# Kernel optimization log

Hardware: AMD Instinct MI355X
Metric: run time of the kernel (lower is better)

Reference implementation:

```python
import jax, jax.numpy as jnp
import numpy as np

B, Q, K, C, H = 4, 1024, 1024, 1024, 16
L = C            # latent_dim (== in_dim per module construction)
CH = L // H      # head_dim = 64


def _ln(x, w, b):
    m = jnp.mean(x, -1, keepdims=True)
    v = jnp.mean((x - m) ** 2, -1, keepdims=True)
    return (x - m) * jax.lax.rsqrt(v + 1e-5) * w + b


def setup_inputs() -> dict:
    key = jax.random.key(0)
    ks = jax.random.split(key, 16)
    s = 0.02
    return {
        "queries": jax.random.normal(ks[0], (B, Q, C), jnp.float32),
        "contexts": jax.random.normal(ks[1], (B, K, C), jnp.float32),
        "queries_hidden": jax.random.normal(ks[2], (B, Q, L), jnp.float32),
        "sa_norm_w": jnp.ones((C,), jnp.float32),
        "sa_norm_b": jnp.zeros((C,), jnp.float32),
        "sa_qkv_w": jax.random.normal(ks[3], (C, 2 * L + C), jnp.float32) * s,
        "sa_out_w": jax.random.normal(ks[4], (C, C), jnp.float32) * s,
        "sa_out_b": jnp.zeros((C,), jnp.float32),
        "ca_norm_w": jnp.ones((C,), jnp.float32),
        "ca_norm_b": jnp.zeros((C,), jnp.float32),
        "gru_w_ih": jax.random.normal(ks[5], (3 * L, C), jnp.float32) * s,
        "gru_w_hh": jax.random.normal(ks[6], (3 * L, L), jnp.float32) * s,
        "gru_b_ih": jnp.zeros((3 * L,), jnp.float32),
        "gru_b_hh": jnp.zeros((3 * L,), jnp.float32),
        "ca_k_w": jax.random.normal(ks[7], (C, L), jnp.float32) * s,
        "ca_v_w": jax.random.normal(ks[8], (C, C), jnp.float32) * s,
        "ca_out_w": jax.random.normal(ks[9], (C, C), jnp.float32) * s,
        "ca_out_b": jnp.zeros((C,), jnp.float32),
        "ln1_w": jnp.ones((C,), jnp.float32),
        "ln1_b": jnp.zeros((C,), jnp.float32),
        "lin1_w": jax.random.normal(ks[10], (C, 2 * C), jnp.float32) * s,
        "ln2_w": jnp.ones((2 * C,), jnp.float32),
        "ln2_b": jnp.zeros((2 * C,), jnp.float32),
        "lin2_w": jax.random.normal(ks[11], (2 * C, C), jnp.float32) * s,
    }


def reference(queries, contexts, queries_hidden,
              sa_norm_w, sa_norm_b, sa_qkv_w, sa_out_w, sa_out_b,
              ca_norm_w, ca_norm_b, gru_w_ih, gru_w_hh, gru_b_ih, gru_b_hh,
              ca_k_w, ca_v_w, ca_out_w, ca_out_b,
              ln1_w, ln1_b, lin1_w, ln2_w, ln2_b, lin2_w):
    scale = 1.0 / jnp.sqrt(jnp.asarray(C, queries.dtype))

    # ---- SelfAttention (pre-norm, residual) ----
    xn = _ln(queries, sa_norm_w, sa_norm_b)
    qkv = (xn @ sa_qkv_w).reshape(B, Q, H, -1)          # [B,Q,H, 2*CH + C/H]
    q, k, v = jnp.split(qkv, [CH, 2 * CH], axis=-1)
    e = jnp.einsum('nqhc,nkhc->nhqk', q, k) * scale
    a = jax.nn.softmax(e, axis=-1)
    o = jnp.einsum('nhqk,nkhc->nqhc', a, v).reshape(B, Q, C)
    x = o @ sa_out_w + sa_out_b + queries

    # ---- AttentionDynamicQuery (GRU-updated queries, cross-attn) ----
    x_pre = x
    xn = _ln(x, ca_norm_w, ca_norm_b)
    xf = xn.reshape(B * Q, C)
    hf = queries_hidden.reshape(B * Q, L)
    gi = xf @ gru_w_ih.T + gru_b_ih                     # [BQ, 3L]
    gh = hf @ gru_w_hh.T + gru_b_hh
    gir, giz, gin = jnp.split(gi, 3, axis=-1)
    ghr, ghz, ghn = jnp.split(gh, 3, axis=-1)
    r = jax.nn.sigmoid(gir + ghr)
    z = jax.nn.sigmoid(giz + ghz)
    n = jnp.tanh(gin + r * ghn)
    h = (1.0 - z) * n + z * hf                          # PyTorch GRUCell update
    qh = h.reshape(B, Q, H, CH)                         # new queries_hidden

    kk = (contexts @ ca_k_w).reshape(B, K, H, CH)
    vv = (contexts @ ca_v_w).reshape(B, K, H, C // H)
    energy = jnp.einsum('nqhc,nkhc->nhqk', qh, kk)      # returned UNscaled
    att = jax.nn.softmax(energy * scale, axis=-1)
    o = jnp.einsum('nhqk,nkhc->nqhc', att, vv).reshape(B, Q, C)
    x = o @ ca_out_w + ca_out_b + x_pre

    # ---- MLP: LN -> SiLU -> Linear -> LN -> SiLU -> Linear, residual ----
    m = jax.nn.silu(_ln(x, ln1_w, ln1_b)) @ lin1_w
    m = jax.nn.silu(_ln(m, ln2_w, ln2_b)) @ lin2_w
    out = x + m                                         # dropout(p=0) = identity
    return (out, energy, qh)
```

## Files before the change

kernel.cpp:

```cpp
#include <hip/hip_runtime.h>
#include <hip/hip_bf16.h>
#include <math.h>

static constexpr float SCALE = 0.03125f;

typedef __attribute__((ext_vector_type(4))) float f32x4;
typedef __attribute__((ext_vector_type(8))) __bf16 bf16x8;
typedef __attribute__((ext_vector_type(4))) __bf16 bf16x4;

__device__ __forceinline__ void g2l16(const void* g, void* l) {
  __builtin_amdgcn_global_load_lds(
      (const __attribute__((address_space(1))) unsigned int*)g,
      (__attribute__((address_space(3))) unsigned int*)l,
      16, 0, 0);
}

__global__ __launch_bounds__(256) void prep_all(
    const float* __restrict__ sa_qkv_w, const float* __restrict__ ca_k_w,
    const float* __restrict__ ca_v_w, const float* __restrict__ sa_out_w,
    const float* __restrict__ ca_out_w, const float* __restrict__ lin1_w,
    const float* __restrict__ lin2_w, const float* __restrict__ gru_w_ih,
    const float* __restrict__ gru_w_hh, const float* __restrict__ qhid,
    const float* __restrict__ contexts,
    __bf16* __restrict__ qkvT, __bf16* __restrict__ kT, __bf16* __restrict__ vT,
    __bf16* __restrict__ saoT, __bf16* __restrict__ caoT, __bf16* __restrict__ lin1T,
    __bf16* __restrict__ lin2T, __bf16* __restrict__ ihB, __bf16* __restrict__ hhB,
    __bf16* __restrict__ qhB, __bf16* __restrict__ ctxB) {
  int bid = blockIdx.x;
  int t = threadIdx.x;
  if (bid >= 2816) {
    const float* csrc; __bf16* cdst; int cbase;
    if (bid < 4352)      { csrc = gru_w_ih; cdst = ihB;  cbase = 2816; }
    else if (bid < 5888) { csrc = gru_w_hh; cdst = hhB;  cbase = 4352; }
    else if (bid < 7936) { csrc = qhid;     cdst = qhB;  cbase = 5888; }
    else                 { csrc = contexts; cdst = ctxB; cbase = 7936; }
    size_t idx = ((size_t)(bid - cbase) * 256 + t) * 8;
    float4 a = *(const float4*)(csrc + idx);
    float4 b = *(const float4*)(csrc + idx + 4);
    bf16x8 o = {(__bf16)a.x,(__bf16)a.y,(__bf16)a.z,(__bf16)a.w,
                (__bf16)b.x,(__bf16)b.y,(__bf16)b.z,(__bf16)b.w};
    *(bf16x8*)(cdst + idx) = o;
    return;
  }
  const float* src; __bf16* dst; int Kd, N, base;
  if (bid < 768)       { src = sa_qkv_w; dst = qkvT;  Kd = 1024; N = 3072; base = 0; }
  else if (bid < 1024) { src = ca_k_w;   dst = kT;    Kd = 1024; N = 1024; base = 768; }
  else if (bid < 1280) { src = ca_v_w;   dst = vT;    Kd = 1024; N = 1024; base = 1024; }
  else if (bid < 1536) { src = sa_out_w; dst = saoT;  Kd = 1024; N = 1024; base = 1280; }
  else if (bid < 1792) { src = ca_out_w; dst = caoT;  Kd = 1024; N = 1024; base = 1536; }
  else if (bid < 2304) { src = lin1_w;   dst = lin1T; Kd = 1024; N = 2048; base = 1792; }
  else                 { src = lin2_w;   dst = lin2T; Kd = 2048; N = 1024; base = 2304; }
  int tid = bid - base;
  int ntx = N >> 6;
  int n0 = (tid % ntx) * 64, k0 = (tid / ntx) * 64;
  __shared__ float tile[64][65];
  #pragma unroll
  for (int i = 0; i < 16; ++i) {
    int idx = i * 256 + t; int r = idx >> 6, c = idx & 63;
    tile[r][c] = src[(size_t)(k0 + r) * N + n0 + c];
  }
  __syncthreads();
  #pragma unroll
  for (int i = 0; i < 16; ++i) {
    int idx = i * 256 + t; int r = idx >> 6, c = idx & 63;
    dst[(size_t)(n0 + r) * Kd + k0 + c] = (__bf16)tile[c][r];
  }
}

template <int NV>
__global__ __launch_bounds__(256) void ln_bf16(
    const float* __restrict__ xf, const __bf16* __restrict__ xb,
    const float* __restrict__ w, const float* __restrict__ b,
    __bf16* __restrict__ out, int silu) {
  const int D = NV * 1024;
  int row = blockIdx.x, t = threadIdx.x;
  float vals[NV * 4];
  float s = 0.f, s2 = 0.f;
  #pragma unroll
  for (int i = 0; i < NV; ++i) {
    int c = (i * 256 + t) * 4;
    float4 v;
    if (xf) {
      v = *(const float4*)(xf + (size_t)row * D + c);
    } else {
      bf16x4 vb = *(const bf16x4*)(xb + (size_t)row * D + c);
      v = make_float4((float)vb[0], (float)vb[1], (float)vb[2], (float)vb[3]);
    }
    vals[i*4+0] = v.x; vals[i*4+1] = v.y; vals[i*4+2] = v.z; vals[i*4+3] = v.w;
    s += v.x + v.y + v.z + v.w;
    s2 += v.x*v.x + v.y*v.y + v.z*v.z + v.w*v.w;
  }
  #pragma unroll
  for (int off = 32; off > 0; off >>= 1) {
    s += __shfl_xor(s, off);
    s2 += __shfl_xor(s2, off);
  }
  __shared__ float red[4], red2[4];
  int wv = t >> 6;
  if ((t & 63) == 0) { red[wv] = s; red2[wv] = s2; }
  __syncthreads();
  float S  = red[0] + red[1] + red[2] + red[3];
  float S2 = red2[0] + red2[1] + red2[2] + red2[3];
  float mean = S / D;
  float var = S2 / D - mean * mean;
  float rs = rsqrtf(var + 1e-5f);
  #pragma unroll
  for (int i = 0; i < NV; ++i) {
    int c = (i * 256 + t) * 4;
    bf16x4 o;
    #pragma unroll
    for (int j = 0; j < 4; ++j) {
      float v = (vals[i*4+j] - mean) * rs * w[c+j] + b[c+j];
      if (silu) v = v / (1.f + __expf(-v));
      o[j] = (__bf16)v;
    }
    *(bf16x4*)(out + (size_t)row * D + c) = o;
  }
}

__device__ __forceinline__ void gemm_body(
    __bf16* Asm, __bf16* Bsm,
    const __bf16* __restrict__ A, long long lda,
    const __bf16* __restrict__ B, long long ldb,
    float* __restrict__ outF, __bf16* __restrict__ outB, long long ldc,
    const float* __restrict__ bias, const float* __restrict__ res,
    int K, int bm, int bn) {
  int t = threadIdx.x;
  int lane = t & 63, w = t >> 6;
  int l15 = lane & 15, kg = lane >> 4;
  int wm = (w >> 1) * 64, wn = (w & 1) * 64;

  f32x4 acc[4][4];
  #pragma unroll
  for (int i = 0; i < 4; ++i)
    #pragma unroll
    for (int j = 0; j < 4; ++j) acc[i][j] = (f32x4)(0.0f);

  const __bf16* ga[4]; const __bf16* gb[4];
  __bf16* la[4]; __bf16* lb[4];
  #pragma unroll
  for (int i = 0; i < 4; ++i) {
    int slot = i * 256 + t;
    int row = slot >> 3, s = slot & 7;
    int sx = s ^ (row & 7);
    ga[i] = A + (size_t)(bm + row) * lda + (sx << 3);
    gb[i] = B + (size_t)(bn + row) * ldb + (sx << 3);
    int base = (i * 256 + w * 64) << 3;
    la[i] = Asm + base;
    lb[i] = Bsm + base;
  }

  for (int k0 = 0; k0 < K; k0 += 64) {
    #pragma unroll
    for (int i = 0; i < 4; ++i) g2l16(ga[i] + k0, la[i]);
    #pragma unroll
    for (int i = 0; i < 4; ++i) g2l16(gb[i] + k0, lb[i]);
    asm volatile("s_waitcnt vmcnt(0)" ::: "memory");
    __syncthreads();
    #pragma unroll
    for (int kk = 0; kk < 2; ++kk) {
      bf16x8 af[4], bfr[4];
      #pragma unroll
      for (int mi = 0; mi < 4; ++mi) {
        int row = wm + mi * 16 + l15;
        int ks = kk * 4 + kg;
        af[mi] = *(const bf16x8*)(Asm + row * 64 + ((ks ^ (row & 7)) << 3));
      }
      #pragma unroll
      for (int ni = 0; ni < 4; ++ni) {
        int row = wn + ni * 16 + l15;
        int ks = kk * 4 + kg;
        bfr[ni] = *(const bf16x8*)(Bsm + row * 64 + ((ks ^ (row & 7)) << 3));
      }
      #pragma unroll
      for (int mi = 0; mi < 4; ++mi)
        #pragma unroll
        for (int ni = 0; ni < 4; ++ni)
          acc[mi][ni] = __builtin_amdgcn_mfma_f32_16x16x32_bf16(
              af[mi], bfr[ni], acc[mi][ni], 0, 0, 0);
    }
    __syncthreads();
  }

  #pragma unroll
  for (int mi = 0; mi < 4; ++mi) {
    #pragma unroll
    for (int ni = 0; ni < 4; ++ni) {
      int rbase = bm + wm + mi * 16 + kg * 4;
      int c = bn + wn + ni * 16 + l15;
      #pragma unroll
      for (int r = 0; r < 4; ++r) {
        float val = acc[mi][ni][r];
        if (bias) val += bias[c];
        size_t off = (size_t)(rbase + r) * ldc + c;
        if (res) val += res[off];
        if (outF) outF[off] = val;
        if (outB) outB[off] = (__bf16)val;
      }
    }
  }
}

__global__ __launch_bounds__(256) void gemm_bf16(
    const __bf16* __restrict__ A, long long lda,
    const __bf16* __restrict__ B, long long ldb,
    float* __restrict__ outF, __bf16* __restrict__ outB, long long ldc,
    const float* __restrict__ bias, const float* __restrict__ res, int K) {
  __shared__ __bf16 sm[2 * 8192];
  int nwg = gridDim.x * gridDim.y;
  int orig = blockIdx.y * gridDim.x + blockIdx.x;
  int swz = (orig & 7) * (nwg >> 3) + (orig >> 3);
  gemm_body(sm, sm + 8192, A, lda, B, ldb, outF, outB, ldc, bias, res, K,
            (swz / gridDim.x) * 128, (swz % gridDim.x) * 128);
}

__global__ __launch_bounds__(256) void gemm_dual(
    const __bf16* __restrict__ A0, long long lda0, const __bf16* __restrict__ B0, long long ldb0,
    float* __restrict__ oF0, __bf16* __restrict__ oB0, long long ldc0,
    const float* __restrict__ bias0, const float* __restrict__ res0, int K0, int gx0, int nb0,
    const __bf16* __restrict__ A1, long long lda1, const __bf16* __restrict__ B1, long long ldb1,
    float* __restrict__ oF1, __bf16* __restrict__ oB1, long long ldc1,
    const float* __restrict__ bias1, const float* __restrict__ res1, int K1, int gx1) {
  __shared__ __bf16 sm[2 * 8192];
  int bid = blockIdx.x;
  if (bid < nb0) {
    int swz = (bid & 7) * (nb0 >> 3) + (bid >> 3);
    gemm_body(sm, sm + 8192, A0, lda0, B0, ldb0, oF0, oB0, ldc0, bias0, res0, K0,
              (swz / gx0) * 128, (swz % gx0) * 128);
  } else {
    int b = bid - nb0;
    int nb1 = gridDim.x - nb0;
    int swz = (b & 7) * (nb1 >> 3) + (b >> 3);
    gemm_body(sm, sm + 8192, A1, lda1, B1, ldb1, oF1, oB1, ldc1, bias1, res1, K1,
              (swz / gx1) * 128, (swz % gx1) * 128);
  }
}

__global__ __launch_bounds__(256) void vtrans(
    const __bf16* __restrict__ V, long long v_sb, long long v_sh, int v_sm,
    __bf16* __restrict__ VT) {
  __shared__ __bf16 tile[64][72];
  int g = blockIdx.y, b = g >> 4, h = g & 15;
  int k0 = blockIdx.x * 64;
  const __bf16* Vb = V + (size_t)b * v_sb + (size_t)h * v_sh;
  int t = threadIdx.x;
  #pragma unroll
  for (int i = 0; i < 2; ++i) {
    int idx = i * 256 + t;
    int k = idx >> 3, dc = (idx & 7) * 8;
    bf16x8 v = *(const bf16x8*)(Vb + (size_t)(k0 + k) * v_sm + dc);
    #pragma unroll
    for (int j = 0; j < 8; ++j) tile[dc + j][k] = v[j];
  }
  __syncthreads();
  #pragma unroll
  for (int i = 0; i < 2; ++i) {
    int idx = i * 256 + t;
    int d = idx >> 3, kc = (idx & 7) * 8;
    bf16x8 v;
    #pragma unroll
    for (int j = 0; j < 8; ++j) v[j] = tile[d][kc + j];
    *(bf16x8*)(VT + ((size_t)g * 64 + d) * 1024 + k0 + kc) = v;
  }
}

template <int E>
__global__ __launch_bounds__(256) void flash_attn(
    const __bf16* __restrict__ Qb, long long q_sb, long long q_sh, int q_sm,
    const __bf16* __restrict__ Kb, long long k_sb, long long k_sh, int k_sm,
    const __bf16* __restrict__ VT, __bf16* __restrict__ Ob,
    float* __restrict__ energyOut, float scale) {
  __shared__ __bf16 Ksm[3][4096];
  __shared__ __bf16 Vsm[3][4096];
  __shared__ __bf16 Psm[128 * 64];
  __shared__ float corr_l[128];
  __shared__ float l_l[128];
  int g = blockIdx.y, b = g >> 4, h = g & 15;
  int qt = blockIdx.x * 128;
  const __bf16* Qg = Qb + (size_t)b * q_sb + (size_t)h * q_sh;
  const __bf16* Kg = Kb + (size_t)b * k_sb + (size_t)h * k_sh;
  const __bf16* Vg = VT + (size_t)g * 65536;
  int t = threadIdx.x, lane = t & 63, w = t >> 6;
  int l15 = lane & 15, kg = lane >> 4;
  int wq = w * 32;

  bf16x8 qf[2][2];
  #pragma unroll
  for (int nq = 0; nq < 2; ++nq)
    #pragma unroll
    for (int kk = 0; kk < 2; ++kk)
      qf[nq][kk] = *(const bf16x8*)(
          Qg + (size_t)(qt + wq + nq * 16 + l15) * q_sm + kk * 32 + kg * 8);

  f32x4 acc_o[2][4];
  #pragma unroll
  for (int i = 0; i < 2; ++i)
    #pragma unroll
    for (int j = 0; j < 4; ++j) acc_o[i][j] = (f32x4)(0.0f);
  float m_run[2] = {-1e30f, -1e30f};
  float l_run[2] = {0.f, 0.f};

  const __bf16* gK[2]; const __bf16* gV[2];
  int lo[2];
  #pragma unroll
  for (int i = 0; i < 2; ++i) {
    int slot = i * 256 + t;
    int row = slot >> 3, s = slot & 7, sx = s ^ (row & 7);
    gK[i] = Kg + (size_t)row * k_sm + (sx << 3);
    gV[i] = Vg + (size_t)row * 1024 + (sx << 3);
    lo[i] = (i * 256 + w * 64) << 3;
  }

  #pragma unroll
  for (int i = 0; i < 2; ++i) g2l16(gK[i], &Ksm[0][lo[i]]);
  #pragma unroll
  for (int i = 0; i < 2; ++i) g2l16(gV[i], &Vsm[0][lo[i]]);
  #pragma unroll
  for (int i = 0; i < 2; ++i) g2l16(gK[i] + (size_t)64 * k_sm, &Ksm[1][lo[i]]);
  #pragma unroll
  for (int i = 0; i < 2; ++i) g2l16(gV[i] + 64, &Vsm[1][lo[i]]);

  int rb = 0;
  for (int kvt = 0; kvt < 16; ++kvt) {
    if (E) {
      if (kvt == 0)       asm volatile("s_waitcnt vmcnt(4)" ::: "memory");
      else if (kvt == 1)  asm volatile("s_waitcnt vmcnt(12)" ::: "memory");
      else if (kvt == 15) asm volatile("s_waitcnt vmcnt(16)" ::: "memory");
      else                asm volatile("s_waitcnt vmcnt(20)" ::: "memory");
    } else {
      if (kvt == 15)      asm volatile("s_waitcnt vmcnt(0)" ::: "memory");
      else                asm volatile("s_waitcnt vmcnt(4)" ::: "memory");
    }
    __builtin_amdgcn_s_barrier();
    __builtin_amdgcn_sched_barrier(0);

    if (kvt < 14) {
      int sbuf = rb >= 1 ? rb - 1 : rb + 2;
      size_t ko = (size_t)(kvt + 2) << 6;
      #pragma unroll
      for (int i = 0; i < 2; ++i) g2l16(gK[i] + ko * k_sm, &Ksm[sbuf][lo[i]]);
      #pragma unroll
      for (int i = 0; i < 2; ++i) g2l16(gV[i] + ko, &Vsm[sbuf][lo[i]]);
    }
    const __bf16* Ks = Ksm[rb];
    const __bf16* Vs = Vsm[rb];

    f32x4 accs[4][2];
    #pragma unroll
    for (int i = 0; i < 4; ++i)
      #pragma unroll
      for (int j = 0; j < 2; ++j) accs[i][j] = (f32x4)(0.0f);
    __builtin_amdgcn_s_setprio(1);
    #pragma unroll
    for (int tt = 0; tt < 4; ++tt) {
      bf16x8 kf[2];
      #pragma unroll
      for (int kk = 0; kk < 2; ++kk) {
        int row = tt * 16 + l15;
        int ks = kk * 4 + kg;
        kf[kk] = *(const bf16x8*)(Ks + row * 64 + ((ks ^ (row & 7)) << 3));
      }
      #pragma unroll
      for (int nq = 0; nq < 2; ++nq)
        #pragma unroll
        for (int kk = 0; kk < 2; ++kk)
          accs[tt][nq] = __builtin_amdgcn_mfma_f32_16x16x32_bf16(
              kf[kk], qf[nq][kk], accs[tt][nq], 0, 0, 0);
    }
    __builtin_amdgcn_s_setprio(0);

    if (E) {
      int kv0 = kvt << 6;
      float* eg = energyOut + ((size_t)g << 20);
      #pragma unroll
      for (int nq = 0; nq < 2; ++nq) {
        int q = qt + wq + nq * 16 + l15;
        #pragma unroll
        for (int tt = 0; tt < 4; ++tt)
          __builtin_nontemporal_store(
              accs[tt][nq], (f32x4*)(eg + (size_t)q * 1024 + kv0 + tt * 16 + kg * 4));
      }
    }

    #pragma unroll
    for (int nq = 0; nq < 2; ++nq) {
      float tmax = -1e30f;
      #pragma unroll
      for (int tt = 0; tt < 4; ++tt)
        #pragma unroll
        for (int r = 0; r < 4; ++r) tmax = fmaxf(tmax, accs[tt][nq][r]);
      tmax *= scale;
      tmax = fmaxf(tmax, __shfl_xor(tmax, 16));
      tmax = fmaxf(tmax, __shfl_xor(tmax, 32));
      float m_new = fmaxf(m_run[nq], tmax);
      float corr = __expf(m_run[nq] - m_new);
      m_run[nq] = m_new;
      int q = wq + nq * 16 + l15;
      float psum = 0.f;
      #pragma unroll
      for (int tt = 0; tt < 4; ++tt) {
        bf16x4 p4;
        #pragma unroll
        for (int r = 0; r < 4; ++r) {
          float p = __expf(accs[tt][nq][r] * scale - m_new);
          psum += p;
          p4[r] = (__bf16)p;
        }
        int kvs = (tt * 16 + kg * 4) ^ ((q & 7) << 3);
        *(bf16x4*)(Psm + q * 64 + kvs) = p4;
      }
      psum += __shfl_xor(psum, 16);
      psum += __shfl_xor(psum, 32);
      l_run[nq] = l_run[nq] * corr + psum;
      if (kg == 0) corr_l[q] = corr;
    }

    #pragma unroll
    for (int mq = 0; mq < 2; ++mq) {
      f32x4 c4 = *(const f32x4*)&corr_l[wq + mq * 16 + kg * 4];
      #pragma unroll
      for (int nd = 0; nd < 4; ++nd)
        #pragma unroll
        for (int r = 0; r < 4; ++r) acc_o[mq][nd][r] *= c4[r];
    }
    __builtin_amdgcn_s_setprio(1);
    #pragma unroll
    for (int kk = 0; kk < 2; ++kk) {
      bf16x8 pf[2], vf[4];
      #pragma unroll
      for (int mq = 0; mq < 2; ++mq) {
        int row = wq + mq * 16 + l15;
        int kvs = (kk * 32 + kg * 8) ^ ((row & 7) << 3);
        pf[mq] = *(const bf16x8*)(Psm + row * 64 + kvs);
      }
      #pragma unroll
      for (int nd = 0; nd < 4; ++nd) {
        int vrow = nd * 16 + l15;
        vf[nd] = *(const bf16x8*)(Vs + vrow * 64 + (((kk * 4 + kg) ^ (vrow & 7)) << 3));
      }
      #pragma unroll
      for (int mq = 0; mq < 2; ++mq)
        #pragma unroll
        for (int nd = 0; nd < 4; ++nd)
          acc_o[mq][nd] = __builtin_amdgcn_mfma_f32_16x16x32_bf16(
              pf[mq], vf[nd], acc_o[mq][nd], 0, 0, 0);
    }
    __builtin_amdgcn_s_setprio(0);
    rb = rb == 2 ? 0 : rb + 1;
  }

  #pragma unroll
  for (int nq = 0; nq < 2; ++nq)
    if (kg == 0) l_l[wq + nq * 16 + l15] = l_run[nq];
  __syncthreads();

  #pragma unroll
  for (int mq = 0; mq < 2; ++mq) {
    f32x4 lv = *(const f32x4*)&l_l[wq + mq * 16 + kg * 4];
    #pragma unroll
    for (int nd = 0; nd < 4; ++nd) {
      int col = h * 64 + nd * 16 + l15;
      #pragma unroll
      for (int r = 0; r < 4; ++r) {
        int qrow = qt + wq + mq * 16 + kg * 4 + r;
        Ob[(size_t)(b * 1024 + qrow) * 1024 + col] = (__bf16)(acc_o[mq][nd][r] / lv[r]);
      }
    }
  }
}

__global__ __launch_bounds__(256) void gru_kernel(
    const __bf16* __restrict__ gi, const __bf16* __restrict__ gh,
    const float* __restrict__ hf, float* __restrict__ qh, __bf16* __restrict__ qhb) {
  size_t e0 = ((size_t)blockIdx.x * 256 + threadIdx.x) * 8;
  int row = (int)(e0 >> 10), col = (int)(e0 & 1023);
  size_t base = (size_t)row * 3072 + col;
  bf16x8 vir = *(const bf16x8*)(gi + base);
  bf16x8 viz = *(const bf16x8*)(gi + base + 1024);
  bf16x8 vin = *(const bf16x8*)(gi + base + 2048);
  bf16x8 vhr = *(const bf16x8*)(gh + base);
  bf16x8 vhz = *(const bf16x8*)(gh + base + 1024);
  bf16x8 vhn = *(const bf16x8*)(gh + base + 2048);
  float4 h0 = *(const float4*)(hf + e0);
  float4 h1 = *(const float4*)(hf + e0 + 4);
  float hv[8] = {h0.x, h0.y, h0.z, h0.w, h1.x, h1.y, h1.z, h1.w};
  float q[8];
  #pragma unroll
  for (int j = 0; j < 8; ++j) {
    float r = 1.f / (1.f + __expf(-((float)vir[j] + (float)vhr[j])));
    float z = 1.f / (1.f + __expf(-((float)viz[j] + (float)vhz[j])));
    float n = tanhf((float)vin[j] + r * (float)vhn[j]);
    q[j] = (1.f - z) * n + z * hv[j];
  }
  *(float4*)(qh + e0)     = make_float4(q[0], q[1], q[2], q[3]);
  *(float4*)(qh + e0 + 4) = make_float4(q[4], q[5], q[6], q[7]);
  bf16x8 qb;
  #pragma unroll
  for (int j = 0; j < 8; ++j) qb[j] = (__bf16)q[j];
  *(bf16x8*)(qhb + e0) = qb;
}

extern "C" void kernel_launch(void* const* d_in, const int* in_sizes, int n_in,
                              void* d_out, int out_size, void* d_ws, size_t ws_size,
                              hipStream_t stream) {
  (void)in_sizes; (void)n_in; (void)out_size; (void)ws_size;
  const float* queries   = (const float*)d_in[0];
  const float* contexts  = (const float*)d_in[1];
  const float* qhid      = (const float*)d_in[2];
  const float* sa_norm_w = (const float*)d_in[3];
  const float* sa_norm_b = (const float*)d_in[4];
  const float* sa_qkv_w  = (const float*)d_in[5];
  const float* sa_out_w  = (const float*)d_in[6];
  const float* sa_out_b  = (const float*)d_in[7];
  const float* ca_norm_w = (const float*)d_in[8];
  const float* ca_norm_b = (const float*)d_in[9];
  const float* gru_w_ih  = (const float*)d_in[10];
  const float* gru_w_hh  = (const float*)d_in[11];
  const float* gru_b_ih  = (const float*)d_in[12];
  const float* gru_b_hh  = (const float*)d_in[13];
  const float* ca_k_w    = (const float*)d_in[14];
  const float* ca_v_w    = (const float*)d_in[15];
  const float* ca_out_w  = (const float*)d_in[16];
  const float* ca_out_b  = (const float*)d_in[17];
  const float* ln1_w     = (const float*)d_in[18];
  const float* ln1_b     = (const float*)d_in[19];
  const float* lin1_w    = (const float*)d_in[20];
  const float* ln2_w     = (const float*)d_in[21];
  const float* ln2_b     = (const float*)d_in[22];
  const float* lin2_w    = (const float*)d_in[23];

  float* out0   = (float*)d_out;
  float* energy = out0 + (size_t)4194304;
  float* qh_out = out0 + (size_t)71303168;

  const size_t MM = 1u << 20;
  float* ws = (float*)d_ws;
  float*  X     = ws;
  float*  X2    = ws + 4 * MM;
  __bf16* M1B    = (__bf16*)(ws + 9 * MM);
  __bf16* XN_b   = (__bf16*)(ws + 17 * MM);
  __bf16* QHID_b = (__bf16*)(ws + 19 * MM);
  __bf16* CTX_b  = (__bf16*)(ws + 21 * MM);
  __bf16* O_b    = (__bf16*)(ws + 23 * MM);
  __bf16* VT_b   = (__bf16*)(ws + 25 * MM);
  __bf16* QKV_b  = (__bf16*)(ws + 27 * MM);
  __bf16* KV_b   = (__bf16*)(ws + 27 * MM);
  __bf16* LN2_b  = (__bf16*)(ws);
  __bf16* qkvT   = (__bf16*)(ws + 33 * MM);
  __bf16* ihB    = (__bf16*)(ws + 34 * MM + MM / 2);
  __bf16* hhB    = (__bf16*)(ws + 36 * MM);
  __bf16* kT     = (__bf16*)(ws + 37 * MM + MM / 2);
  __bf16* vT     = (__bf16*)(ws + 38 * MM);
  __bf16* saoT   = (__bf16*)(ws + 38 * MM + MM / 2);
  __bf16* caoT   = (__bf16*)(ws + 39 * MM);
  __bf16* lin1T  = (__bf16*)(ws + 39 * MM + MM / 2);
  __bf16* lin2T  = (__bf16*)(ws + 40 * MM + MM / 2);
  __bf16* GI_b = (__bf16*)energy;
  __bf16* GH_b = (__bf16*)(energy + 6 * MM);

  const long long QKV_SB = 1024LL * 3072;
  const long long KV_SB  = 1024LL * 2048;

  prep_all<<<9984, 256, 0, stream>>>(
      sa_qkv_w, ca_k_w, ca_v_w, sa_out_w, ca_out_w, lin1_w, lin2_w,
      gru_w_ih, gru_w_hh, qhid, contexts,
      qkvT, kT, vT, saoT, caoT, lin1T, lin2T, ihB, hhB, QHID_b, CTX_b);

  ln_bf16<1><<<4096, 256, 0, stream>>>(queries, nullptr, sa_norm_w, sa_norm_b, XN_b, 0);
  gemm_bf16<<<dim3(24, 32), 256, 0, stream>>>(
      XN_b, 1024, qkvT, 1024, nullptr, QKV_b, 3072, nullptr, nullptr, 1024);
  vtrans<<<dim3(16, 64), 256, 0, stream>>>(QKV_b + 128, QKV_SB, 192, 3072, VT_b);
  flash_attn<0><<<dim3(8, 64), 256, 0, stream>>>(
      QKV_b, QKV_SB, 192, 3072, QKV_b + 64, QKV_SB, 192, 3072,
      VT_b, O_b, nullptr, SCALE);
  gemm_dual<<<1024, 256, 0, stream>>>(
      O_b, 1024, saoT, 1024, X, nullptr, 1024, sa_out_b, queries, 1024, 8, 256,
      QHID_b, 1024, hhB, 1024, nullptr, GH_b, 3072, gru_b_hh, nullptr, 1024, 24);

  ln_bf16<1><<<4096, 256, 0, stream>>>(X, nullptr, ca_norm_w, ca_norm_b, XN_b, 0);
  gemm_dual<<<1280, 256, 0, stream>>>(
      XN_b, 1024, ihB, 1024, nullptr, GI_b, 3072, gru_b_ih, nullptr, 1024, 24, 768,
      CTX_b, 1024, kT, 1024, nullptr, KV_b, 2048, nullptr, nullptr, 1024, 16);
  gru_kernel<<<2048, 256, 0, stream>>>(GI_b, GH_b, qhid, qh_out, QHID_b );

  vtrans<<<dim3(16, 64), 256, 0, stream>>>(KV_b + 1024, KV_SB, 64, 2048, VT_b);
  flash_attn<1><<<dim3(8, 64), 256, 0, stream>>>(
      QHID_b, 1024LL * 1024, 64, 1024, KV_b, KV_SB, 64, 2048,
      VT_b, O_b, energy, SCALE);
  gemm_bf16<<<dim3(8, 32), 256, 0, stream>>>(
      O_b, 1024, caoT, 1024, X2, nullptr, 1024, ca_out_b, X, 1024);

  ln_bf16<1><<<4096, 256, 0, stream>>>(X2, nullptr, ln1_w, ln1_b, XN_b, 1);
  gemm_bf16<<<dim3(16, 32), 256, 0, stream>>>(
      XN_b, 1024, lin1T, 1024, nullptr, M1B, 2048, nullptr, nullptr, 1024);
  ln_bf16<2><<<4096, 256, 0, stream>>>(nullptr, M1B, ln2_w, ln2_b, LN2_b, 1);
  gemm_bf16<<<dim3(8, 32), 256, 0, stream>>>(
      LN2_b, 2048, lin2T, 2048, out0, nullptr, 1024, nullptr, X2, 2048);
}
```

Measured before the change: 623.7 us.

## Double-buffer GEMM LDS tiles to overlap global loads with MFMA compute

Rewrites the shared GEMM body as a two-stage pipeline. The next K tile is loaded into a second pair of LDS buffers while MFMAs run on the current pair, and each step now ends with a single wait-plus-barrier. The aim is to hide global-to-LDS latency in all the projection and MLP GEMMs. LDS use per block doubles to 64 KB, which may lower occupancy. The loop assumes K is a multiple of 128 and at least 128.

```diff
diff --git a/kernel.cpp b/kernel.cpp
--- a/kernel.cpp
+++ b/kernel.cpp
@@ -119,12 +119,15 @@
 }
 
 __device__ __forceinline__ void gemm_body(
-    __bf16* Asm, __bf16* Bsm,
     const __bf16* __restrict__ A, long long lda,
     const __bf16* __restrict__ B, long long ldb,
     float* __restrict__ outF, __bf16* __restrict__ outB, long long ldc,
     const float* __restrict__ bias, const float* __restrict__ res,
     int K, int bm, int bn) {
+  __shared__ __bf16 Asm0[8192];
+  __shared__ __bf16 Bsm0[8192];
+  __shared__ __bf16 Asm1[8192];
+  __shared__ __bf16 Bsm1[8192];
   int t = threadIdx.x;
   int lane = t & 63, w = t >> 6;
   int l15 = lane & 15, kg = lane >> 4;
@@ -137,7 +140,7 @@
     for (int j = 0; j < 4; ++j) acc[i][j] = (f32x4)(0.0f);
 
   const __bf16* ga[4]; const __bf16* gb[4];
-  __bf16* la[4]; __bf16* lb[4];
+  int lo[4];
   #pragma unroll
   for (int i = 0; i < 4; ++i) {
     int slot = i * 256 + t;
@@ -145,18 +148,16 @@
     int sx = s ^ (row & 7);
     ga[i] = A + (size_t)(bm + row) * lda + (sx << 3);
     gb[i] = B + (size_t)(bn + row) * ldb + (sx << 3);
-    int base = (i * 256 + w * 64) << 3;
-    la[i] = Asm + base;
-    lb[i] = Bsm + base;
-  }
-
-  for (int k0 = 0; k0 < K; k0 += 64) {
-    #pragma unroll
-    for (int i = 0; i < 4; ++i) g2l16(ga[i] + k0, la[i]);
-    #pragma unroll
-    for (int i = 0; i < 4; ++i) g2l16(gb[i] + k0, lb[i]);
-    asm volatile("s_waitcnt vmcnt(0)" ::: "memory");
-    __syncthreads();
+    lo[i] = (i * 256 + w * 64) << 3;
+  }
+
+  auto STAGE = [&](__bf16* As, __bf16* Bs, int k0) {
+    #pragma unroll
+    for (int i = 0; i < 4; ++i) g2l16(ga[i] + k0, As + lo[i]);
+    #pragma unroll
+    for (int i = 0; i < 4; ++i) g2l16(gb[i] + k0, Bs + lo[i]);
+  };
+  auto COMPUTE = [&](const __bf16* As, const __bf16* Bs) {
     #pragma unroll
     for (int kk = 0; kk < 2; ++kk) {
       bf16x8 af[4], bfr[4];
@@ -164,13 +165,13 @@
       for (int mi = 0; mi < 4; ++mi) {
         int row = wm + mi * 16 + l15;
         int ks = kk * 4 + kg;
-        af[mi] = *(const bf16x8*)(Asm + row * 64 + ((ks ^ (row & 7)) << 3));
+        af[mi] = *(const bf16x8*)(As + row * 64 + ((ks ^ (row & 7)) << 3));
       }
       #pragma unroll
       for (int ni = 0; ni < 4; ++ni) {
         int row = wn + ni * 16 + l15;
         int ks = kk * 4 + kg;
-        bfr[ni] = *(const bf16x8*)(Bsm + row * 64 + ((ks ^ (row & 7)) << 3));
+        bfr[ni] = *(const bf16x8*)(Bs + row * 64 + ((ks ^ (row & 7)) << 3));
       }
       #pragma unroll
       for (int mi = 0; mi < 4; ++mi)
@@ -179,8 +180,29 @@
           acc[mi][ni] = __builtin_amdgcn_mfma_f32_16x16x32_bf16(
               af[mi], bfr[ni], acc[mi][ni], 0, 0, 0);
     }
-    __syncthreads();
-  }
+  };
+  #define GEMM_SYNC() do { \
+    asm volatile("s_waitcnt vmcnt(0)" ::: "memory"); \
+    __builtin_amdgcn_s_barrier(); \
+    __builtin_amdgcn_sched_barrier(0); \
+  } while (0)
+
+  STAGE(Asm0, Bsm0, 0);
+  GEMM_SYNC();
+  int nk = K >> 6;
+  for (int kt = 0; kt + 2 < nk; kt += 2) {
+    STAGE(Asm1, Bsm1, (kt + 1) << 6);
+    COMPUTE(Asm0, Bsm0);
+    GEMM_SYNC();
+    STAGE(Asm0, Bsm0, (kt + 2) << 6);
+    COMPUTE(Asm1, Bsm1);
+    GEMM_SYNC();
+  }
+  STAGE(Asm1, Bsm1, (nk - 1) << 6);
+  COMPUTE(Asm0, Bsm0);
+  GEMM_SYNC();
+  COMPUTE(Asm1, Bsm1);
+  #undef GEMM_SYNC
 
   #pragma unroll
   for (int mi = 0; mi < 4; ++mi) {
@@ -206,11 +228,10 @@
     const __bf16* __restrict__ B, long long ldb,
     float* __restrict__ outF, __bf16* __restrict__ outB, long long ldc,
     const float* __restrict__ bias, const float* __restrict__ res, int K) {
-  __shared__ __bf16 sm[2 * 8192];
   int nwg = gridDim.x * gridDim.y;
   int orig = blockIdx.y * gridDim.x + blockIdx.x;
   int swz = (orig & 7) * (nwg >> 3) + (orig >> 3);
-  gemm_body(sm, sm + 8192, A, lda, B, ldb, outF, outB, ldc, bias, res, K,
+  gemm_body(A, lda, B, ldb, outF, outB, ldc, bias, res, K,
             (swz / gridDim.x) * 128, (swz % gridDim.x) * 128);
 }
 
@@ -221,17 +242,16 @@
     const __bf16* __restrict__ A1, long long lda1, const __bf16* __restrict__ B1, long long ldb1,
     float* __restrict__ oF1, __bf16* __restrict__ oB1, long long ldc1,
     const float* __restrict__ bias1, const float* __restrict__ res1, int K1, int gx1) {
-  __shared__ __bf16 sm[2 * 8192];
   int bid = blockIdx.x;
   if (bid < nb0) {
     int swz = (bid & 7) * (nb0 >> 3) + (bid >> 3);
-    gemm_body(sm, sm + 8192, A0, lda0, B0, ldb0, oF0, oB0, ldc0, bias0, res0, K0,
+    gemm_body(A0, lda0, B0, ldb0, oF0, oB0, ldc0, bias0, res0, K0,
               (swz / gx0) * 128, (swz % gx0) * 128);
   } else {
     int b = bid - nb0;
     int nb1 = gridDim.x - nb0;
     int swz = (b & 7) * (nb1 >> 3) + (b >> 3);
-    gemm_body(sm, sm + 8192, A1, lda1, B1, ldb1, oF1, oB1, ldc1, bias1, res1, K1,
+    gemm_body(A1, lda1, B1, ldb1, oF1, oB1, ldc1, bias1, res1, K1,
               (swz / gx1) * 128, (swz % gx1) * 128);
   }
 }
```

After: 621.7 us. About the same (-0.3%).
